# Optimization experiments

Measured on AMD Instinct MI355X. Metric: run time of the kernel, lower is better.

## Reference

```python
import jax, jax.numpy as jnp
import numpy as np

NUM_LANDMARKS = 256
PINV_ITERS = 6


def iterative_inv(K):
    # Newton-Schulz iterative pseudo-inverse (Nystromformer), K: [B, m, m]
    I = jnp.eye(K.shape[-1], dtype=K.dtype)
    V = K.swapaxes(-1, -2) / (jnp.max(jnp.sum(K, axis=-2)) * jnp.max(jnp.sum(K, axis=-1)))
    for _ in range(PINV_ITERS):
        KV = K @ V
        V = 0.25 * V @ (13.0 * I - KV @ (15.0 * I - KV @ (7.0 * I - KV)))
    return V


def nystrom_attention_matrix(q, k, m):
    # q, k: [B, N, d] -> approximate softmax(q k^T / sqrt(d)) of shape [B, N, N]
    B, N, d = q.shape
    scale = 1.0 / jnp.sqrt(jnp.asarray(d, q.dtype))
    L = N // m
    q_l = q.reshape(B, m, L, d).mean(axis=2)  # landmark queries [B, m, d]
    k_l = k.reshape(B, m, L, d).mean(axis=2)  # landmark keys    [B, m, d]
    k1 = jax.nn.softmax(jnp.einsum('bnd,bmd->bnm', q, k_l) * scale, axis=-1)   # [B, N, m]
    k2 = jax.nn.softmax(jnp.einsum('bld,bmd->blm', q_l, k_l) * scale, axis=-1) # [B, m, m]
    k3 = jax.nn.softmax(jnp.einsum('bmd,bnd->bmn', q_l, k) * scale, axis=-1)   # [B, m, N]
    return (k1 @ iterative_inv(k2)) @ k3  # [B, N, N]


def setup_inputs() -> dict:
    key = jax.random.key(0)
    ks = jax.random.split(key, 8)
    B, C, T, W, H = 2, 64, 4, 32, 32
    d = C // 8
    scale = 0.05  # keep q.k scores in a sane softmax range
    return {
        'x': jax.random.normal(ks[0], (B, C, T, W, H), dtype=jnp.float32),
        'wq': jax.random.normal(ks[1], (d, C), dtype=jnp.float32) * scale,
        'bq': jax.random.normal(ks[2], (d,), dtype=jnp.float32) * scale,
        'wk': jax.random.normal(ks[3], (d, C), dtype=jnp.float32) * scale,
        'bk': jax.random.normal(ks[4], (d,), dtype=jnp.float32) * scale,
        'wv': jax.random.normal(ks[5], (C, C), dtype=jnp.float32) * scale,
        'bv': jax.random.normal(ks[6], (C,), dtype=jnp.float32) * scale,
        'gamma': jax.random.normal(ks[7], (1,), dtype=jnp.float32),
    }


def reference(x, wq, bq, wk, bk, wv, bv, gamma):
    B, C, T, W, H = x.shape
    N = T * W * H
    xf = x.reshape(B, C, N)
    # 1x1x1 Conv3d == per-token linear over channels
    q = jnp.einsum('oc,bcn->bno', wq, xf) + bq            # [B, N, C//8]
    k = jnp.einsum('oc,bcn->bno', wk, xf) + bk            # [B, N, C//8]
    v = jnp.einsum('oc,bcn->bon', wv, xf) + bv[None, :, None]  # [B, C, N]
    attn = nystrom_attention_matrix(q, k, NUM_LANDMARKS)  # [B, N, N]
    # out = bmm(value, attn^T): out[b,c,i] = sum_j v[b,c,j] * attn[b,i,j]
    out = jnp.einsum('bcj,bij->bci', v, attn).reshape(B, C, T, W, H)
    out = gamma[0] * out + x
    return out, attn
```

## Files before the change

### kernel.cpp

```cpp
#include <hip/hip_runtime.h>
#include <hip/hip_bf16.h>
#include <math.h>

#define NB 2
#define NC 64
#define ND 8
#define NN 4096
#define NM 256
#define NL 16
#define SCALE 0.35355339059327373f

typedef __attribute__((ext_vector_type(4))) float f32x4;
typedef __attribute__((ext_vector_type(8))) short bf16x8;

__device__ inline ushort f2bf(float f) {
  __hip_bfloat16 h = __float2bfloat16(f);
  return *reinterpret_cast<ushort*>(&h);
}
__device__ inline float bf2f(ushort u) {
  return __uint_as_float(((unsigned int)u) << 16);
}

__device__ inline void gl_lds16(const void* g, void* l) {
  __builtin_amdgcn_global_load_lds(
      (const __attribute__((address_space(1))) unsigned int*)g,
      (__attribute__((address_space(3))) unsigned int*)l, 16, 0, 0);
}

__global__ __launch_bounds__(256) void qkv2l_kernel(
    const float* __restrict__ x,
    const float* __restrict__ wq, const float* __restrict__ bq,
    const float* __restrict__ wk, const float* __restrict__ bk,
    const float* __restrict__ wv, const float* __restrict__ bv,
    float* __restrict__ q, float* __restrict__ k, float* __restrict__ v,
    float* __restrict__ ql, float* __restrict__ kl) {
  __shared__ float ws[NC];
  int o = blockIdx.x;
  int b = blockIdx.z;
  int n0 = blockIdx.y * 1024;
  int t = threadIdx.x;
  const float* wrow;
  float bias;
  if (o < ND)            { wrow = wq + (size_t)o * NC;            bias = bq[o]; }
  else if (o < 2 * ND)   { wrow = wk + (size_t)(o - ND) * NC;     bias = bk[o - ND]; }
  else                   { wrow = wv + (size_t)(o - 2 * ND) * NC; bias = bv[o - 2 * ND]; }
  if (t < NC) ws[t] = wrow[t];
  __syncthreads();
  int n = n0 + t * 4;
  float4 acc = {bias, bias, bias, bias};
  #pragma unroll
  for (int c = 0; c < NC; ++c) {
    float wc = ws[c];
    float4 xv = *(const float4*)(x + ((size_t)b * NC + c) * NN + n);
    acc.x += wc * xv.x; acc.y += wc * xv.y; acc.z += wc * xv.z; acc.w += wc * xv.w;
  }
  if (o < ND) {
    float* qp = q + ((size_t)b * NN + n) * ND + o;
    qp[0] = acc.x; qp[8] = acc.y; qp[16] = acc.z; qp[24] = acc.w;
  } else if (o < 2 * ND) {
    float* kp = k + ((size_t)b * NN + n) * ND + (o - ND);
    kp[0] = acc.x; kp[8] = acc.y; kp[16] = acc.z; kp[24] = acc.w;
  } else {
    *(float4*)(v + ((size_t)b * NC + (o - 2 * ND)) * NN + n) = acc;
  }
  if (o < 2 * ND) {
    float s4 = acc.x + acc.y + acc.z + acc.w;
    s4 += __shfl_xor(s4, 1);
    s4 += __shfl_xor(s4, 2);
    if ((t & 3) == 0) {
      int g = n0 / 16 + (t >> 2);
      float* dst = (o < ND) ? ql : kl;
      dst[((size_t)b * NM + g) * ND + (o & 7)] = s4 * (1.0f / 16.0f);
    }
  }
}

__global__ __launch_bounds__(256) void scores_all_kernel(
    const float* __restrict__ q, const float* __restrict__ ql,
    const float* __restrict__ kw, const float* __restrict__ kl,
    ushort* __restrict__ k1bf, float* __restrict__ k2w,
    float* __restrict__ k3w) {
  __shared__ float skl[NM][9];
  __shared__ float wred[4], wsum[4];
  int blk = blockIdx.x;
  int t = threadIdx.x;
  if (blk < 2048 + 128) {
    const float* Q; int R, b, xrow;
    bool isbf;
    if (blk < 2048) { b = blk >> 10; xrow = blk & 1023; Q = q;  R = NN; isbf = true; }
    else { int r = blk - 2048; b = r >> 6; xrow = r & 63; Q = ql; R = NM; isbf = false; }
    for (int i = t; i < NM * ND; i += 256) skl[i >> 3][i & 7] = kl[(size_t)b * NM * ND + i];
    __syncthreads();
    int wave = t >> 6, lane = t & 63;
    int r = xrow * 4 + wave;
    const float* qrow = Q + ((size_t)b * R + r) * ND;
    float qr[ND];
    #pragma unroll
    for (int dd = 0; dd < ND; ++dd) qr[dd] = qrow[dd];
    float sc[4];
    float lmax = -1e30f;
    #pragma unroll
    for (int s = 0; s < 4; ++s) {
      int j = lane + 64 * s;
      float a = 0.f;
      #pragma unroll
      for (int dd = 0; dd < ND; ++dd) a += qr[dd] * skl[j][dd];
      sc[s] = a * SCALE;
      lmax = fmaxf(lmax, sc[s]);
    }
    for (int off = 32; off; off >>= 1) lmax = fmaxf(lmax, __shfl_xor(lmax, off));
    float lsum = 0.f;
    #pragma unroll
    for (int s = 0; s < 4; ++s) { sc[s] = expf(sc[s] - lmax); lsum += sc[s]; }
    for (int off = 32; off; off >>= 1) lsum += __shfl_xor(lsum, off);
    float inv = 1.0f / lsum;
    if (isbf) {
      #pragma unroll
      for (int s = 0; s < 4; ++s)
        k1bf[((size_t)b * R + r) * NM + lane + 64 * s] = f2bf(sc[s] * inv);
    } else {
      #pragma unroll
      for (int s = 0; s < 4; ++s)
        k2w[((size_t)b * R + r) * NM + lane + 64 * s] = sc[s] * inv;
    }
  } else {
    int r = blk - 2176;
    int b = r >> 8, i = r & 255;
    float qr[ND];
    #pragma unroll
    for (int dd = 0; dd < ND; ++dd) qr[dd] = ql[((size_t)b * NM + i) * ND + dd];
    float sc[16];
    float lmax = -1e30f;
    #pragma unroll
    for (int s = 0; s < 16; ++s) {
      int n = t + 256 * s;
      const float* kp = kw + ((size_t)b * NN + n) * ND;
      float a = 0.f;
      #pragma unroll
      for (int dd = 0; dd < ND; ++dd) a += qr[dd] * kp[dd];
      sc[s] = a * SCALE;
      lmax = fmaxf(lmax, sc[s]);
    }
    for (int off = 32; off; off >>= 1) lmax = fmaxf(lmax, __shfl_xor(lmax, off));
    if ((t & 63) == 0) wred[t >> 6] = lmax;
    __syncthreads();
    lmax = fmaxf(fmaxf(wred[0], wred[1]), fmaxf(wred[2], wred[3]));
    float lsum = 0.f;
    #pragma unroll
    for (int s = 0; s < 16; ++s) { sc[s] = expf(sc[s] - lmax); lsum += sc[s]; }
    for (int off = 32; off; off >>= 1) lsum += __shfl_xor(lsum, off);
    if ((t & 63) == 0) wsum[t >> 6] = lsum;
    __syncthreads();
    lsum = wsum[0] + wsum[1] + wsum[2] + wsum[3];
    float inv = 1.0f / lsum;
    #pragma unroll
    for (int s = 0; s < 16; ++s) k3w[((size_t)b * NM + i) * NN + t + 256 * s] = sc[s] * inv;
  }
}

__global__ __launch_bounds__(256) void denom_kernel(const float* __restrict__ k2,
                                                    float* __restrict__ denw) {
  __shared__ float red[256];
  int b = blockIdx.x;
  int t = threadIdx.x;
  float cs = 0.f;
  for (int i = 0; i < NM; ++i) cs += k2[((size_t)b * NM + i) * NM + t];
  red[t] = cs;
  __syncthreads();
  for (int off = 128; off; off >>= 1) {
    if (t < off) red[t] = fmaxf(red[t], red[t + off]);
    __syncthreads();
  }
  if (t == 0) denw[b] = red[0];
}

__global__ void vinit_kernel(const float* __restrict__ k2, const float* __restrict__ denw,
                             float* __restrict__ V) {
  int idx = blockIdx.x * 256 + threadIdx.x;
  int b = idx / (NM * NM), r = idx % (NM * NM), i = r / NM, j = r % NM;
  float dval = 1.0f / fmaxf(denw[0], denw[1]);
  V[idx] = k2[((size_t)b * NM + j) * NM + i] * dval;
}

__global__ __launch_bounds__(256) void gemm_rk32(
    const float* __restrict__ A, const float* __restrict__ Bm,
    float* __restrict__ out, float s_a, float s_ab) {
  int b = blockIdx.z;
  int bi = blockIdx.y * 32, bj = blockIdx.x * 32;
  __shared__ float As[32][260];
  __shared__ float Bs[256][36];
  int t = threadIdx.x;
  const float* Ab = A + (size_t)b * NM * NM;
  const float* Bb = Bm + (size_t)b * NM * NM;
  #pragma unroll
  for (int q = 0; q < 8; ++q) {
    int s = q * 256 + t;
    int ar = s >> 6, ac = (s & 63) * 4;
    *(float4*)&As[ar][ac] = *(const float4*)(Ab + (size_t)(bi + ar) * NM + ac);
    int br = s >> 3, bc = (s & 7) * 4;
    *(float4*)&Bs[br][bc] = *(const float4*)(Bb + (size_t)br * NM + bj + bc);
  }
  __syncthreads();
  int tx = t & 15, ty = t >> 4;
  float acc[2][2] = {};
  #pragma unroll 8
  for (int kk = 0; kk < NM; ++kk) {
    float a0 = As[ty * 2][kk], a1 = As[ty * 2 + 1][kk];
    float b0 = Bs[kk][tx * 2], b1 = Bs[kk][tx * 2 + 1];
    acc[0][0] += a0 * b0; acc[0][1] += a0 * b1;
    acc[1][0] += a1 * b0; acc[1][1] += a1 * b1;
  }
  #pragma unroll
  for (int i = 0; i < 2; ++i)
    #pragma unroll
    for (int j = 0; j < 2; ++j) {
      size_t o = ((size_t)b * NM + bi + ty * 2 + i) * NM + bj + tx * 2 + j;
      float r = s_ab * acc[i][j];
      if (s_a != 0.0f) r += s_a * A[o];
      out[o] = r;
    }
}

__global__ __launch_bounds__(256) void cvt_vinv_kernel(const float* __restrict__ Va,
                                                       ushort* __restrict__ Vt) {
  int b = blockIdx.z;
  int n0 = blockIdx.x * 32, m0 = blockIdx.y * 32;
  __shared__ float tile[32][33];
  int t = threadIdx.x;
  int r = t >> 3, c4 = (t & 7) * 4;
  float4 v = *(const float4*)(Va + ((size_t)b * NM + m0 + r) * NM + n0 + c4);
  tile[c4][r] = v.x; tile[c4 + 1][r] = v.y; tile[c4 + 2][r] = v.z; tile[c4 + 3][r] = v.w;
  __syncthreads();
  ushort4 u;
  u.x = f2bf(tile[r][c4]);     u.y = f2bf(tile[r][c4 + 1]);
  u.z = f2bf(tile[r][c4 + 2]); u.w = f2bf(tile[r][c4 + 3]);
  *(ushort4*)(Vt + ((size_t)b * NM + n0 + r) * NM + m0 + c4) = u;
}

__global__ __launch_bounds__(256) void cvt_t_kernel(const float* __restrict__ k3,
                                                    ushort* __restrict__ k3t) {
  int b = blockIdx.z;
  int n0 = blockIdx.x * 32, m0 = blockIdx.y * 32;
  __shared__ float tile[32][33];
  int t = threadIdx.x;
  int r = t >> 3, c4 = (t & 7) * 4;
  float4 v = *(const float4*)(k3 + ((size_t)b * NM + m0 + r) * NN + n0 + c4);
  tile[c4][r] = v.x; tile[c4 + 1][r] = v.y; tile[c4 + 2][r] = v.z; tile[c4 + 3][r] = v.w;
  __syncthreads();
  ushort4 u;
  u.x = f2bf(tile[r][c4]);     u.y = f2bf(tile[r][c4 + 1]);
  u.z = f2bf(tile[r][c4 + 2]); u.w = f2bf(tile[r][c4 + 3]);
  *(ushort4*)(k3t + ((size_t)b * NN + n0 + r) * NM + m0 + c4) = u;
}

__global__ __launch_bounds__(256) void gemm_a_mfma(
    const ushort* __restrict__ k1bf, const ushort* __restrict__ Vt,
    ushort* __restrict__ Abf) {
  int b = blockIdx.z;
  int bi = blockIdx.y * 128, bj = blockIdx.x * 128;
  __shared__ ushort As[128 * 64];
  __shared__ ushort Bs[128 * 64];
  int t = threadIdx.x;
  int wave = t >> 6, lane = t & 63;
  int wr = wave >> 1, wc = wave & 1;
  const ushort* Ab = k1bf + (size_t)b * NN * NM;
  const ushort* Bb = Vt + (size_t)b * NM * NM;
  f32x4 acc[4][4] = {};
  for (int k0 = 0; k0 < NM; k0 += 64) {
    #pragma unroll
    for (int q = 0; q < 4; ++q) {
      int s = q * 256 + t;
      int r = s >> 3, c = s & 7;
      int cs = (c ^ (r & 7)) << 3;
      gl_lds16(Ab + (size_t)(bi + r) * NM + k0 + cs, As + (size_t)s * 8);
      gl_lds16(Bb + (size_t)(bj + r) * NM + k0 + cs, Bs + (size_t)s * 8);
    }
    __syncthreads();
    #pragma unroll
    for (int kk = 0; kk < 2; ++kk) {
      int koff = kk * 64 + (lane >> 4) * 16;
      bf16x8 af[4], bfv[4];
      #pragma unroll
      for (int mi = 0; mi < 4; ++mi) {
        int row = wr * 64 + mi * 16 + (lane & 15);
        af[mi] = *(const bf16x8*)((const char*)As + row * 128 + (koff ^ ((row & 7) << 4)));
      }
      #pragma unroll
      for (int nj = 0; nj < 4; ++nj) {
        int row = wc * 64 + nj * 16 + (lane & 15);
        bfv[nj] = *(const bf16x8*)((const char*)Bs + row * 128 + (koff ^ ((row & 7) << 4)));
      }
      #pragma unroll
      for (int mi = 0; mi < 4; ++mi)
        #pragma unroll
        for (int nj = 0; nj < 4; ++nj)
          acc[mi][nj] = __builtin_amdgcn_mfma_f32_16x16x32_bf16(af[mi], bfv[nj], acc[mi][nj], 0, 0, 0);
    }
    __syncthreads();
  }
  int col = lane & 15, rbase = (lane >> 4) * 4;
  #pragma unroll
  for (int mi = 0; mi < 4; ++mi)
    #pragma unroll
    for (int nj = 0; nj < 4; ++nj)
      #pragma unroll
      for (int r = 0; r < 4; ++r)
        Abf[((size_t)b * NN + bi + wr * 64 + mi * 16 + rbase + r) * NM
            + bj + wc * 64 + nj * 16 + col] = f2bf(acc[mi][nj][r]);
}

__global__ __launch_bounds__(256) void gemm_attn_mfma(
    const ushort* __restrict__ Abf, const ushort* __restrict__ K3T,
    float* __restrict__ attn) {
  int lin = blockIdx.z * 1024 + blockIdx.y * 32 + blockIdx.x;
  int swz = (lin & 7) * 256 + (lin >> 3);
  int b = swz >> 10;
  int rem = swz & 1023;
  int bi = (rem >> 5) * 128, bj = (rem & 31) * 128;
  __shared__ ushort As[128 * 64];
  __shared__ ushort Bs[128 * 64];
  int t = threadIdx.x;
  int wave = t >> 6, lane = t & 63;
  int wr = wave >> 1, wc = wave & 1;
  const ushort* Ab = Abf + (size_t)b * NN * NM;
  const ushort* Bb = K3T + (size_t)b * NN * NM;
  f32x4 acc[4][4] = {};
  for (int k0 = 0; k0 < NM; k0 += 64) {
    #pragma unroll
    for (int q = 0; q < 4; ++q) {
      int s = q * 256 + t;
      int r = s >> 3, c = s & 7;
      int cs = (c ^ (r & 7)) << 3;
      gl_lds16(Ab + (size_t)(bi + r) * NM + k0 + cs, As + (size_t)s * 8);
      gl_lds16(Bb + (size_t)(bj + r) * NM + k0 + cs, Bs + (size_t)s * 8);
    }
    __syncthreads();
    #pragma unroll
    for (int kk = 0; kk < 2; ++kk) {
      int koff = kk * 64 + (lane >> 4) * 16;
      bf16x8 af[4], bfv[4];
      #pragma unroll
      for (int mi = 0; mi < 4; ++mi) {
        int row = wr * 64 + mi * 16 + (lane & 15);
        af[mi] = *(const bf16x8*)((const char*)As + row * 128 + (koff ^ ((row & 7) << 4)));
      }
      #pragma unroll
      for (int nj = 0; nj < 4; ++nj) {
        int row = wc * 64 + nj * 16 + (lane & 15);
        bfv[nj] = *(const bf16x8*)((const char*)Bs + row * 128 + (koff ^ ((row & 7) << 4)));
      }
      #pragma unroll
      for (int mi = 0; mi < 4; ++mi)
        #pragma unroll
        for (int nj = 0; nj < 4; ++nj)
          acc[mi][nj] = __builtin_amdgcn_mfma_f32_16x16x32_bf16(af[mi], bfv[nj], acc[mi][nj], 0, 0, 0);
    }
    __syncthreads();
  }
  int col = lane & 15, rbase = (lane >> 4) * 4;
  #pragma unroll
  for (int mi = 0; mi < 4; ++mi)
    #pragma unroll
    for (int nj = 0; nj < 4; ++nj)
      #pragma unroll
      for (int r = 0; r < 4; ++r)
        __builtin_nontemporal_store(
            acc[mi][nj][r],
            &attn[((size_t)b * NN + bi + wr * 64 + mi * 16 + rbase + r) * NN
                  + bj + wc * 64 + nj * 16 + col]);
}

__global__ __launch_bounds__(256) void kv_kernel(
    const float* __restrict__ K3, const float* __restrict__ Vv,
    float* __restrict__ kvout) {
  int b = blockIdx.z, bp = blockIdx.x * 64;
  int j0base = blockIdx.y * (NN / 32);
  __shared__ float Ks[64][33], Vs[64][33];
  int t = threadIdx.x, tx = t & 15, ty = t >> 4;
  int lrow = t >> 2, ljc = (t & 3) * 8;
  float acc[4][4] = {};
  for (int j0 = j0base; j0 < j0base + NN / 32; j0 += 32) {
    float4 a0 = *(const float4*)(K3 + ((size_t)b * NM + bp + lrow) * NN + j0 + ljc);
    float4 a1 = *(const float4*)(K3 + ((size_t)b * NM + bp + lrow) * NN + j0 + ljc + 4);
    float4 v0 = *(const float4*)(Vv + ((size_t)b * NC + lrow) * NN + j0 + ljc);
    float4 v1 = *(const float4*)(Vv + ((size_t)b * NC + lrow) * NN + j0 + ljc + 4);
    Ks[lrow][ljc + 0] = a0.x; Ks[lrow][ljc + 1] = a0.y; Ks[lrow][ljc + 2] = a0.z; Ks[lrow][ljc + 3] = a0.w;
    Ks[lrow][ljc + 4] = a1.x; Ks[lrow][ljc + 5] = a1.y; Ks[lrow][ljc + 6] = a1.z; Ks[lrow][ljc + 7] = a1.w;
    Vs[lrow][ljc + 0] = v0.x; Vs[lrow][ljc + 1] = v0.y; Vs[lrow][ljc + 2] = v0.z; Vs[lrow][ljc + 3] = v0.w;
    Vs[lrow][ljc + 4] = v1.x; Vs[lrow][ljc + 5] = v1.y; Vs[lrow][ljc + 6] = v1.z; Vs[lrow][ljc + 7] = v1.w;
    __syncthreads();
    #pragma unroll
    for (int kk = 0; kk < 32; ++kk) {
      float av_[4], bv_[4];
      #pragma unroll
      for (int i = 0; i < 4; ++i) av_[i] = Ks[(ty << 2) + i][kk];
      #pragma unroll
      for (int j = 0; j < 4; ++j) bv_[j] = Vs[(tx << 2) + j][kk];
      #pragma unroll
      for (int i = 0; i < 4; ++i)
        #pragma unroll
        for (int j = 0; j < 4; ++j) acc[i][j] += av_[i] * bv_[j];
    }
    __syncthreads();
  }
  #pragma unroll
  for (int i = 0; i < 4; ++i)
    #pragma unroll
    for (int j = 0; j < 4; ++j)
      atomicAdd(&kvout[((size_t)b * NM + bp + (ty << 2) + i) * NC + (tx << 2) + j], acc[i][j]);
}

__global__ __launch_bounds__(256) void out_kernel(
    const ushort* __restrict__ Abf, const float* __restrict__ kvm,
    const float* __restrict__ x, const float* __restrict__ gamma,
    float* __restrict__ outp) {
  __shared__ float As[32 * 256];
  int blk = blockIdx.x;
  int b = blk / (NN / 32), n0 = (blk % (NN / 32)) * 32;
  int t = threadIdx.x;
  for (int it = 0; it < 32; ++it)
    As[it * 256 + (t ^ (it & 31))] = bf2f(Abf[((size_t)b * NN + n0 + it) * NM + t]);
  __syncthreads();
  int tn = t & 31, cg0 = (t >> 5) * 8;
  float g = gamma[0];
  float acc[8] = {};
  for (int p = 0; p < NM; ++p) {
    float a = As[tn * 256 + (p ^ (tn & 31))];
    float4 kv0 = *(const float4*)(kvm + ((size_t)b * NM + p) * NC + cg0);
    float4 kv1 = *(const float4*)(kvm + ((size_t)b * NM + p) * NC + cg0 + 4);
    acc[0] += a * kv0.x; acc[1] += a * kv0.y; acc[2] += a * kv0.z; acc[3] += a * kv0.w;
    acc[4] += a * kv1.x; acc[5] += a * kv1.y; acc[6] += a * kv1.z; acc[7] += a * kv1.w;
  }
  #pragma unroll
  for (int qd = 0; qd < 8; ++qd) {
    int c = cg0 + qd;
    size_t idx = ((size_t)b * NC + c) * NN + n0 + tn;
    __builtin_nontemporal_store(g * acc[qd] + x[idx], &outp[idx]);
  }
}

extern "C" void kernel_launch(void* const* d_in, const int* in_sizes, int n_in,
                              void* d_out, int out_size, void* d_ws, size_t ws_size,
                              hipStream_t stream) {
  const float* x     = (const float*)d_in[0];
  const float* wq    = (const float*)d_in[1];
  const float* bq    = (const float*)d_in[2];
  const float* wk    = (const float*)d_in[3];
  const float* bk    = (const float*)d_in[4];
  const float* wv    = (const float*)d_in[5];
  const float* bv    = (const float*)d_in[6];
  const float* gamma = (const float*)d_in[7];
  float* outp = (float*)d_out;
  float* attn = outp + (size_t)NB * NC * NN;
  float* w = (float*)d_ws;

  float* qw   = w;
  float* kw   = qw + 65536;
  float* vw   = kw + 65536;
  float* qlw  = vw + 524288;
  float* klw  = qlw + 4096;
  float* k1w  = klw + 4096;
  float* k2w  = k1w + 2097152;
  float* k3w  = k2w + 131072;
  float* Abuf = k3w + 2097152;
  float* Va   = Abuf + 1048576;
  float* Vb   = Va + 131072;
  float* Zb   = Vb + 131072;
  float* T1   = Zb + 131072;
  float* T2   = T1 + 131072;
  float* Vtw  = T2 + 131072;
  float* kvw  = Vtw + 65536;
  float* denw = kvw + 32768;
  ushort* k1bf  = (ushort*)k1w;
  ushort* k3T   = (ushort*)k1w + 2097152;
  ushort* Abf   = (ushort*)Abuf;
  ushort* Vinvt = (ushort*)Vtw;

  hipMemsetAsync(kvw, 0, (size_t)NB * NM * NC * sizeof(float), stream);
  qkv2l_kernel<<<dim3(80, NN / 1024, NB), dim3(256), 0, stream>>>(
      x, wq, bq, wk, bk, wv, bv, qw, kw, vw, qlw, klw);
  scores_all_kernel<<<dim3(2048 + 128 + 512), dim3(256), 0, stream>>>(
      qw, qlw, kw, klw, k1bf, k2w, k3w);
  denom_kernel<<<dim3(NB), dim3(256), 0, stream>>>(k2w, denw);
  vinit_kernel<<<dim3(NB * NM * NM / 256), dim3(256), 0, stream>>>(k2w, denw, Va);

  float* Vc = Va; float* Vn = Vb;
  for (int it = 0; it < 6; ++it) {
    gemm_rk32<<<dim3(8, 8, NB), dim3(256), 0, stream>>>(k2w, Vc, Zb, 0.f, 1.f);
    gemm_rk32<<<dim3(8, 8, NB), dim3(256), 0, stream>>>(Zb, Zb, T1, 7.f, -1.f);
    gemm_rk32<<<dim3(8, 8, NB), dim3(256), 0, stream>>>(Zb, T1, T2, 15.f, -1.f);
    gemm_rk32<<<dim3(8, 8, NB), dim3(256), 0, stream>>>(Vc, T2, Vn, 3.25f, -0.25f);
    float* tmp = Vc; Vc = Vn; Vn = tmp;
  }

  cvt_vinv_kernel<<<dim3(NM / 32, NM / 32, NB), dim3(256), 0, stream>>>(Vc, Vinvt);
  cvt_t_kernel<<<dim3(NN / 32, NM / 32, NB), dim3(256), 0, stream>>>(k3w, k3T);
  gemm_a_mfma<<<dim3(NM / 128, NN / 128, NB), dim3(256), 0, stream>>>(k1bf, Vinvt, Abf);
  gemm_attn_mfma<<<dim3(NN / 128, NN / 128, NB), dim3(256), 0, stream>>>(Abf, k3T, attn);
  kv_kernel<<<dim3(NM / 64, 32, NB), dim3(256), 0, stream>>>(k3w, vw, kvw);
  out_kernel<<<dim3(NB * NN / 32), dim3(256), 0, stream>>>(Abf, kvw, x, gamma, outp);
}
```

Baseline: 302.0 us.

## Fuse V init and final transpose-convert into Newton-Schulz GEMMs; widen QKV blocks

```diff
diff --git a/kernel.cpp b/kernel.cpp
--- a/kernel.cpp
+++ b/kernel.cpp
@@ -27,50 +27,66 @@
       (__attribute__((address_space(3))) unsigned int*)l, 16, 0, 0);
 }
 
-__global__ __launch_bounds__(256) void qkv2l_kernel(
+__global__ __launch_bounds__(256) void qkv4_kernel(
     const float* __restrict__ x,
     const float* __restrict__ wq, const float* __restrict__ bq,
     const float* __restrict__ wk, const float* __restrict__ bk,
     const float* __restrict__ wv, const float* __restrict__ bv,
     float* __restrict__ q, float* __restrict__ k, float* __restrict__ v,
     float* __restrict__ ql, float* __restrict__ kl) {
-  __shared__ float ws[NC];
-  int o = blockIdx.x;
+  __shared__ float ws[4][NC];
+  int o0 = blockIdx.x * 4;
   int b = blockIdx.z;
   int n0 = blockIdx.y * 1024;
   int t = threadIdx.x;
-  const float* wrow;
-  float bias;
-  if (o < ND)            { wrow = wq + (size_t)o * NC;            bias = bq[o]; }
-  else if (o < 2 * ND)   { wrow = wk + (size_t)(o - ND) * NC;     bias = bk[o - ND]; }
-  else                   { wrow = wv + (size_t)(o - 2 * ND) * NC; bias = bv[o - 2 * ND]; }
-  if (t < NC) ws[t] = wrow[t];
+  {
+    int j = t >> 6, c = t & 63;
+    int o = o0 + j;
+    const float* wrow;
+    if (o < ND)          wrow = wq + (size_t)o * NC;
+    else if (o < 2 * ND) wrow = wk + (size_t)(o - ND) * NC;
+    else                 wrow = wv + (size_t)(o - 2 * ND) * NC;
+    ws[j][c] = wrow[c];
+  }
   __syncthreads();
   int n = n0 + t * 4;
-  float4 acc = {bias, bias, bias, bias};
-  #pragma unroll
+  float4 acc[4];
+  #pragma unroll
+  for (int j = 0; j < 4; ++j) {
+    int o = o0 + j;
+    float bias = (o < ND) ? bq[o] : (o < 2 * ND ? bk[o - ND] : bv[o - 2 * ND]);
+    acc[j].x = bias; acc[j].y = bias; acc[j].z = bias; acc[j].w = bias;
+  }
   for (int c = 0; c < NC; ++c) {
-    float wc = ws[c];
     float4 xv = *(const float4*)(x + ((size_t)b * NC + c) * NN + n);
-    acc.x += wc * xv.x; acc.y += wc * xv.y; acc.z += wc * xv.z; acc.w += wc * xv.w;
-  }
-  if (o < ND) {
-    float* qp = q + ((size_t)b * NN + n) * ND + o;
-    qp[0] = acc.x; qp[8] = acc.y; qp[16] = acc.z; qp[24] = acc.w;
-  } else if (o < 2 * ND) {
-    float* kp = k + ((size_t)b * NN + n) * ND + (o - ND);
-    kp[0] = acc.x; kp[8] = acc.y; kp[16] = acc.z; kp[24] = acc.w;
-  } else {
-    *(float4*)(v + ((size_t)b * NC + (o - 2 * ND)) * NN + n) = acc;
-  }
-  if (o < 2 * ND) {
-    float s4 = acc.x + acc.y + acc.z + acc.w;
-    s4 += __shfl_xor(s4, 1);
-    s4 += __shfl_xor(s4, 2);
-    if ((t & 3) == 0) {
-      int g = n0 / 16 + (t >> 2);
-      float* dst = (o < ND) ? ql : kl;
-      dst[((size_t)b * NM + g) * ND + (o & 7)] = s4 * (1.0f / 16.0f);
+    #pragma unroll
+    for (int j = 0; j < 4; ++j) {
+      float wc = ws[j][c];
+      acc[j].x += wc * xv.x; acc[j].y += wc * xv.y;
+      acc[j].z += wc * xv.z; acc[j].w += wc * xv.w;
+    }
+  }
+  #pragma unroll
+  for (int j = 0; j < 4; ++j) {
+    int o = o0 + j;
+    if (o < ND) {
+      float* qp = q + ((size_t)b * NN + n) * ND + o;
+      qp[0] = acc[j].x; qp[8] = acc[j].y; qp[16] = acc[j].z; qp[24] = acc[j].w;
+    } else if (o < 2 * ND) {
+      float* kp = k + ((size_t)b * NN + n) * ND + (o - ND);
+      kp[0] = acc[j].x; kp[8] = acc[j].y; kp[16] = acc[j].z; kp[24] = acc[j].w;
+    } else {
+      *(float4*)(v + ((size_t)b * NC + (o - 2 * ND)) * NN + n) = acc[j];
+    }
+    if (o < 2 * ND) {
+      float s4 = acc[j].x + acc[j].y + acc[j].z + acc[j].w;
+      s4 += __shfl_xor(s4, 1);
+      s4 += __shfl_xor(s4, 2);
+      if ((t & 3) == 0) {
+        int g = n0 / 16 + (t >> 2);
+        float* dst = (o < ND) ? ql : kl;
+        dst[((size_t)b * NM + g) * ND + (o & 7)] = s4 * (1.0f / 16.0f);
+      }
     }
   }
 }
@@ -174,14 +190,6 @@
   if (t == 0) denw[b] = red[0];
 }
 
-__global__ void vinit_kernel(const float* __restrict__ k2, const float* __restrict__ denw,
-                             float* __restrict__ V) {
-  int idx = blockIdx.x * 256 + threadIdx.x;
-  int b = idx / (NM * NM), r = idx % (NM * NM), i = r / NM, j = r % NM;
-  float dval = 1.0f / fmaxf(denw[0], denw[1]);
-  V[idx] = k2[((size_t)b * NM + j) * NM + i] * dval;
-}
-
 __global__ __launch_bounds__(256) void gemm_rk32(
     const float* __restrict__ A, const float* __restrict__ Bm,
     float* __restrict__ out, float s_a, float s_ab) {
@@ -221,20 +229,128 @@
     }
 }
 
-__global__ __launch_bounds__(256) void cvt_vinv_kernel(const float* __restrict__ Va,
-                                                       ushort* __restrict__ Vt) {
+__global__ __launch_bounds__(256) void gemm_rk32_zv0(
+    const float* __restrict__ k2, const float* __restrict__ denw,
+    float* __restrict__ out) {
   int b = blockIdx.z;
-  int n0 = blockIdx.x * 32, m0 = blockIdx.y * 32;
-  __shared__ float tile[32][33];
-  int t = threadIdx.x;
-  int r = t >> 3, c4 = (t & 7) * 4;
-  float4 v = *(const float4*)(Va + ((size_t)b * NM + m0 + r) * NM + n0 + c4);
-  tile[c4][r] = v.x; tile[c4 + 1][r] = v.y; tile[c4 + 2][r] = v.z; tile[c4 + 3][r] = v.w;
-  __syncthreads();
+  int bi = blockIdx.y * 32, bj = blockIdx.x * 32;
+  __shared__ float As[32][260];
+  __shared__ float Bs[256][36];
+  int t = threadIdx.x;
+  const float* Ab = k2 + (size_t)b * NM * NM;
+  float dval = 1.0f / fmaxf(denw[0], denw[1]);
+  #pragma unroll
+  for (int q = 0; q < 8; ++q) {
+    int s = q * 256 + t;
+    int ar = s >> 6, ac = (s & 63) * 4;
+    *(float4*)&As[ar][ac] = *(const float4*)(Ab + (size_t)(bi + ar) * NM + ac);
+    int br = s >> 6, bk4 = (s & 63) * 4;
+    float4 vv = *(const float4*)(Ab + (size_t)(bj + br) * NM + bk4);
+    Bs[bk4 + 0][br] = vv.x * dval; Bs[bk4 + 1][br] = vv.y * dval;
+    Bs[bk4 + 2][br] = vv.z * dval; Bs[bk4 + 3][br] = vv.w * dval;
+  }
+  __syncthreads();
+  int tx = t & 15, ty = t >> 4;
+  float acc[2][2] = {};
+  #pragma unroll 8
+  for (int kk = 0; kk < NM; ++kk) {
+    float a0 = As[ty * 2][kk], a1 = As[ty * 2 + 1][kk];
+    float b0 = Bs[kk][tx * 2], b1 = Bs[kk][tx * 2 + 1];
+    acc[0][0] += a0 * b0; acc[0][1] += a0 * b1;
+    acc[1][0] += a1 * b0; acc[1][1] += a1 * b1;
+  }
+  #pragma unroll
+  for (int i = 0; i < 2; ++i)
+    #pragma unroll
+    for (int j = 0; j < 2; ++j)
+      out[((size_t)b * NM + bi + ty * 2 + i) * NM + bj + tx * 2 + j] = acc[i][j];
+}
+
+__global__ __launch_bounds__(256) void gemm_rk32_av0(
+    const float* __restrict__ k2, const float* __restrict__ T2,
+    const float* __restrict__ denw, float* __restrict__ out) {
+  int b = blockIdx.z;
+  int bi = blockIdx.y * 32, bj = blockIdx.x * 32;
+  __shared__ float As[32][260];
+  __shared__ float Bs[256][36];
+  int t = threadIdx.x;
+  const float* k2b = k2 + (size_t)b * NM * NM;
+  const float* Bb = T2 + (size_t)b * NM * NM;
+  float dval = 1.0f / fmaxf(denw[0], denw[1]);
+  #pragma unroll
+  for (int q = 0; q < 8; ++q) {
+    int s = q * 256 + t;
+    int kr = s >> 3, c4 = (s & 7) * 4;
+    float4 vv = *(const float4*)(k2b + (size_t)kr * NM + bi + c4);
+    As[c4 + 0][kr] = vv.x * dval; As[c4 + 1][kr] = vv.y * dval;
+    As[c4 + 2][kr] = vv.z * dval; As[c4 + 3][kr] = vv.w * dval;
+    int br = s >> 3, bc = (s & 7) * 4;
+    *(float4*)&Bs[br][bc] = *(const float4*)(Bb + (size_t)br * NM + bj + bc);
+  }
+  __syncthreads();
+  int tx = t & 15, ty = t >> 4;
+  float acc[2][2] = {};
+  #pragma unroll 8
+  for (int kk = 0; kk < NM; ++kk) {
+    float a0 = As[ty * 2][kk], a1 = As[ty * 2 + 1][kk];
+    float b0 = Bs[kk][tx * 2], b1 = Bs[kk][tx * 2 + 1];
+    acc[0][0] += a0 * b0; acc[0][1] += a0 * b1;
+    acc[1][0] += a1 * b0; acc[1][1] += a1 * b1;
+  }
+  #pragma unroll
+  for (int i = 0; i < 2; ++i)
+    #pragma unroll
+    for (int j = 0; j < 2; ++j) {
+      int R = bi + ty * 2 + i, C = bj + tx * 2 + j;
+      float a0v = k2b[(size_t)C * NM + R] * dval;
+      out[((size_t)b * NM + R) * NM + C] = 3.25f * a0v - 0.25f * acc[i][j];
+    }
+}
+
+__global__ __launch_bounds__(256) void gemm_rk32_wt(
+    const float* __restrict__ A, const float* __restrict__ Bm,
+    ushort* __restrict__ Vt) {
+  int b = blockIdx.z;
+  int bi = blockIdx.y * 32, bj = blockIdx.x * 32;
+  __shared__ float As[32][260];
+  __shared__ float Bs[256][36];
+  int t = threadIdx.x;
+  const float* Ab = A + (size_t)b * NM * NM;
+  const float* Bb = Bm + (size_t)b * NM * NM;
+  #pragma unroll
+  for (int q = 0; q < 8; ++q) {
+    int s = q * 256 + t;
+    int ar = s >> 6, ac = (s & 63) * 4;
+    *(float4*)&As[ar][ac] = *(const float4*)(Ab + (size_t)(bi + ar) * NM + ac);
+    int br = s >> 3, bc = (s & 7) * 4;
+    *(float4*)&Bs[br][bc] = *(const float4*)(Bb + (size_t)br * NM + bj + bc);
+  }
+  __syncthreads();
+  int tx = t & 15, ty = t >> 4;
+  float acc[2][2] = {};
+  #pragma unroll 8
+  for (int kk = 0; kk < NM; ++kk) {
+    float a0 = As[ty * 2][kk], a1 = As[ty * 2 + 1][kk];
+    float b0 = Bs[kk][tx * 2], b1 = Bs[kk][tx * 2 + 1];
+    acc[0][0] += a0 * b0; acc[0][1] += a0 * b1;
+    acc[1][0] += a1 * b0; acc[1][1] += a1 * b1;
+  }
+  __syncthreads();
+  float (*tile)[33] = (float (*)[33])&As[0][0];
+  #pragma unroll
+  for (int i = 0; i < 2; ++i)
+    #pragma unroll
+    for (int j = 0; j < 2; ++j) {
+      int R = ty * 2 + i, C = tx * 2 + j;
+      float a0v = Ab[(size_t)(bi + R) * NM + bj + C];
+      tile[R][C] = 3.25f * a0v - 0.25f * acc[i][j];
+    }
+  __syncthreads();
+  int rr = t >> 3, m4 = (t & 7) * 4;
   ushort4 u;
-  u.x = f2bf(tile[r][c4]);     u.y = f2bf(tile[r][c4 + 1]);
-  u.z = f2bf(tile[r][c4 + 2]); u.w = f2bf(tile[r][c4 + 3]);
-  *(ushort4*)(Vt + ((size_t)b * NM + n0 + r) * NM + m0 + c4) = u;
+  u.x = f2bf(tile[m4 + 0][rr]); u.y = f2bf(tile[m4 + 1][rr]);
+  u.z = f2bf(tile[m4 + 2][rr]); u.w = f2bf(tile[m4 + 3][rr]);
+  *(ushort4*)(Vt + ((size_t)b * NM + bj + rr) * NM + bi + m4) = u;
 }
 
 __global__ __launch_bounds__(256) void cvt_t_kernel(const float* __restrict__ k3,
@@ -477,23 +593,29 @@
   ushort* Vinvt = (ushort*)Vtw;
 
   hipMemsetAsync(kvw, 0, (size_t)NB * NM * NC * sizeof(float), stream);
-  qkv2l_kernel<<<dim3(80, NN / 1024, NB), dim3(256), 0, stream>>>(
+  qkv4_kernel<<<dim3(20, NN / 1024, NB), dim3(256), 0, stream>>>(
       x, wq, bq, wk, bk, wv, bv, qw, kw, vw, qlw, klw);
   scores_all_kernel<<<dim3(2048 + 128 + 512), dim3(256), 0, stream>>>(
       qw, qlw, kw, klw, k1bf, k2w, k3w);
   denom_kernel<<<dim3(NB), dim3(256), 0, stream>>>(k2w, denw);
-  vinit_kernel<<<dim3(NB * NM * NM / 256), dim3(256), 0, stream>>>(k2w, denw, Va);
-
+
+  gemm_rk32_zv0<<<dim3(8, 8, NB), dim3(256), 0, stream>>>(k2w, denw, Zb);
+  gemm_rk32<<<dim3(8, 8, NB), dim3(256), 0, stream>>>(Zb, Zb, T1, 7.f, -1.f);
+  gemm_rk32<<<dim3(8, 8, NB), dim3(256), 0, stream>>>(Zb, T1, T2, 15.f, -1.f);
+  gemm_rk32_av0<<<dim3(8, 8, NB), dim3(256), 0, stream>>>(k2w, T2, denw, Va);
   float* Vc = Va; float* Vn = Vb;
-  for (int it = 0; it < 6; ++it) {
+  for (int it = 1; it < 5; ++it) {
     gemm_rk32<<<dim3(8, 8, NB), dim3(256), 0, stream>>>(k2w, Vc, Zb, 0.f, 1.f);
     gemm_rk32<<<dim3(8, 8, NB), dim3(256), 0, stream>>>(Zb, Zb, T1, 7.f, -1.f);
     gemm_rk32<<<dim3(8, 8, NB), dim3(256), 0, stream>>>(Zb, T1, T2, 15.f, -1.f);
     gemm_rk32<<<dim3(8, 8, NB), dim3(256), 0, stream>>>(Vc, T2, Vn, 3.25f, -0.25f);
     float* tmp = Vc; Vc = Vn; Vn = tmp;
   }
-
-  cvt_vinv_kernel<<<dim3(NM / 32, NM / 32, NB), dim3(256), 0, stream>>>(Vc, Vinvt);
+  gemm_rk32<<<dim3(8, 8, NB), dim3(256), 0, stream>>>(k2w, Vc, Zb, 0.f, 1.f);
+  gemm_rk32<<<dim3(8, 8, NB), dim3(256), 0, stream>>>(Zb, Zb, T1, 7.f, -1.f);
+  gemm_rk32<<<dim3(8, 8, NB), dim3(256), 0, stream>>>(Zb, T1, T2, 15.f, -1.f);
+  gemm_rk32_wt<<<dim3(8, 8, NB), dim3(256), 0, stream>>>(Vc, T2, Vinvt);
+
   cvt_t_kernel<<<dim3(NN / 32, NM / 32, NB), dim3(256), 0, stream>>>(k3w, k3T);
   gemm_a_mfma<<<dim3(NM / 128, NN / 128, NB), dim3(256), 0, stream>>>(k1bf, Vinvt, Abf);
   gemm_attn_mfma<<<dim3(NN / 128, NN / 128, NB), dim3(256), 0, stream>>>(Abf, k3T, attn);
```

After: 299.1 us. No clear change (-1.0%).
